# Kernel tuning notes

Measured on AMD Instinct MI355X. Metric: run time of the kernel, lower is better.

Reference implementation:

```python
import jax, jax.numpy as jnp
import numpy as np

NUM_TREES = 32
NUM_NODES = 6
SEED = 0
BATCH, CH, T = 16, 128, 4096


def _make_forest(num_trees, num_nodes, seed):
    """Random rooted trees: node 0 is root, node i>0 attaches to a uniform
    random earlier node (classic random recursive tree). Returns, per tree,
    the children-list representation."""
    rng = np.random.default_rng(seed)
    forest = []
    for _ in range(num_trees):
        children = [[] for _ in range(num_nodes)]
        for i in range(1, num_nodes):
            p = int(rng.integers(0, i))
            children[p].append(i)
        forest.append(children)
    return forest


def _excl_cumsum(u):
    # sum_{s < t} u[..., s]  (exclusive prefix sum along the ordered axis)
    return jnp.cumsum(u, axis=-1) - u


def _sum_trees(x, alphas, forest):
    """Iterated-sums evaluation over a forest in the (plus, times) semiring.
    Node value: v_i(t) = alpha_i * x(t) * prod_{c in children(i)} sum_{s<t} v_c(s).
    Tree output: sum_t v_root(t), per channel. x: [B,C,T]. Returns [B,num_trees,C]."""
    outs = []
    for t_idx, children in enumerate(forest):
        vals = {}
        for i in reversed(range(len(children))):  # leaves-to-root order
            v = alphas[t_idx, i][None, :, None] * x  # [B,C,T]
            for c in children[i]:
                v = v * _excl_cumsum(vals.pop(c))
            vals[i] = v
        outs.append(jnp.sum(vals[0], axis=-1))  # [B,C]
    return jnp.stack(outs, axis=1)  # [B,num_trees,C]


def setup_inputs() -> dict:
    key = jax.random.key(0)
    k1, k2 = jax.random.split(key)
    x = jax.random.normal(k1, (BATCH, CH, T), dtype=jnp.float32)
    alphas = jax.random.normal(k2, (NUM_TREES, NUM_NODES, CH), dtype=jnp.float32)
    return {"x": x, "alphas": alphas}


def reference(x, alphas):
    forest = _make_forest(NUM_TREES, NUM_NODES, SEED)
    return _sum_trees(x, alphas, forest)
```

## Files before the change

kernel.cpp:

```cpp
#include <hip/hip_runtime.h>
#include <cstdint>
#include <cstddef>

namespace cx {

constexpr uint32_t hashmix(uint32_t value, uint32_t& hc) {
    value ^= hc; hc *= 0x931e8875u; value *= hc; value ^= value >> 16; return value;
}
constexpr uint32_t mixf(uint32_t x, uint32_t y) {
    uint32_t r = x * 0xca01f9ddu - y * 0x4973f715u; r ^= r >> 16; return r;
}

struct Pcg64 {
    unsigned __int128 state{}, inc{};
    bool has_uint32{}; uint32_t uinteger{};
    static constexpr unsigned __int128 mult() {
        return (((unsigned __int128)2549297995355413924ULL) << 64) | 4865540595714422341ULL;
    }
    constexpr void step() { state = state * mult() + inc; }
    constexpr void seed_default0() {
        uint32_t pool[4] = {0, 0, 0, 0};
        uint32_t hc = 0x43b0d7e5u;
        for (int i = 0; i < 4; ++i) pool[i] = hashmix(0u, hc);
        for (int isrc = 0; isrc < 4; ++isrc)
            for (int idst = 0; idst < 4; ++idst)
                if (isrc != idst) pool[idst] = mixf(pool[idst], hashmix(pool[isrc], hc));
        uint32_t st[8] = {};
        uint32_t hc2 = 0x8b51f9ddu;
        for (int i = 0; i < 8; ++i) {
            uint32_t dv = pool[i & 3];
            dv ^= hc2; hc2 *= 0x58f38dedu; dv *= hc2; dv ^= dv >> 16;
            st[i] = dv;
        }
        const uint64_t v0 = (uint64_t)st[0] | ((uint64_t)st[1] << 32);
        const uint64_t v1 = (uint64_t)st[2] | ((uint64_t)st[3] << 32);
        const uint64_t v2 = (uint64_t)st[4] | ((uint64_t)st[5] << 32);
        const uint64_t v3 = (uint64_t)st[6] | ((uint64_t)st[7] << 32);
        const unsigned __int128 s = (((unsigned __int128)v0) << 64) | v1;
        const unsigned __int128 i_ = (((unsigned __int128)v2) << 64) | v3;
        state = 0; inc = (i_ << 1) | 1;
        step(); state += s; step();
        has_uint32 = false; uinteger = 0;
    }
    constexpr uint64_t next64() {
        step();
        const uint64_t hi = (uint64_t)(state >> 64), lo = (uint64_t)state;
        const uint64_t x = hi ^ lo;
        const unsigned rot = (unsigned)(state >> 122);
        return (x >> rot) | (x << ((64u - rot) & 63u));
    }
    constexpr uint32_t next32() {
        if (has_uint32) { has_uint32 = false; return uinteger; }
        const uint64_t n = next64();
        has_uint32 = true; uinteger = (uint32_t)(n >> 32);
        return (uint32_t)n;
    }
    constexpr uint32_t bounded_lemire32(uint32_t rng) {
        const uint32_t rng_excl = rng + 1u;
        uint64_t m = (uint64_t)next32() * (uint64_t)rng_excl;
        uint32_t leftover = (uint32_t)m;
        if (leftover < rng_excl) {
            const uint32_t threshold = (0xFFFFFFFFu - rng) % rng_excl;
            while (leftover < threshold) {
                m = (uint64_t)next32() * (uint64_t)rng_excl;
                leftover = (uint32_t)m;
            }
        }
        return (uint32_t)(m >> 32);
    }
    constexpr int64_t integers0(int64_t high) {
        const uint64_t rng = (uint64_t)(high - 1);
        if (rng == 0) return 0;
        return (int64_t)bounded_lemire32((uint32_t)rng);
    }
};

constexpr int NTREE = 32, MAXSER = 32, MAXROOT = 32, MAXFAC = 5, MAXSLOT = 12;

struct Plan {
    int nser, nroot, nslot, maxlvl;
    int lvl[MAXSER];
    int slot[MAXSER];
    int nfac[MAXSER];
    int fac[MAXSER][4];
    int rnfac[MAXROOT];
    int rfac[MAXROOT][MAXFAC];
    int rlvl[MAXROOT];
    int tree_root[NTREE];
};

constexpr Plan build_plan() {
    Plan P{};
    unsigned skey[MAXSER] = {}, rkey[MAXROOT] = {};
    P.nser = 1; skey[0] = (2u << 16) | 2u;
    P.nfac[0] = 0;
    P.nroot = 0;

    Pcg64 rng; rng.seed_default0();
    for (int t = 0; t < NTREE; ++t) {
        int par[6] = {0, 0, 0, 0, 0, 0};
        for (int i = 1; i <= 5; ++i) par[i] = (int)rng.integers0(i);
        int ch[6][5] = {}; int nch[6] = {};
        for (int i = 1; i <= 5; ++i) ch[par[i]][nch[par[i]]++] = i;

        int sid[6] = {}; unsigned keyn[6] = {};
        for (int i = 5; i >= 1; --i) {
            const int n = nch[i];
            unsigned ck[5] = {}; int cf[5] = {};
            for (int k = 0; k < n; ++k) { ck[k] = keyn[ch[i][k]]; cf[k] = sid[ch[i][k]]; }
            for (int a = 0; a < n; ++a)
                for (int bq = a + 1; bq < n; ++bq) {
                    if (ck[bq] > ck[a]) { unsigned tmp = ck[a]; ck[a] = ck[bq]; ck[bq] = tmp; }
                    if (cf[bq] < cf[a]) { int tmp = cf[a]; cf[a] = cf[bq]; cf[bq] = tmp; }
                }
            unsigned bits = 1u, len = 1u;
            for (int k = 0; k < n; ++k) { bits = (bits << (ck[k] >> 16)) | (ck[k] & 0xffffu); len += ck[k] >> 16; }
            bits <<= 1; len += 1;
            const unsigned key = (len << 16) | bits;
            keyn[i] = key;
            int id = -1;
            for (int q = 0; q < P.nser; ++q) if (skey[q] == key) { id = q; break; }
            if (id < 0) {
                id = P.nser++;
                skey[id] = key; P.nfac[id] = n;
                for (int k = 0; k < n; ++k) P.fac[id][k] = cf[k];
            }
            sid[i] = id;
        }
        {
            const int n = nch[0];
            unsigned ck[5] = {}; int cf[5] = {};
            for (int k = 0; k < n; ++k) { ck[k] = keyn[ch[0][k]]; cf[k] = sid[ch[0][k]]; }
            for (int a = 0; a < n; ++a)
                for (int bq = a + 1; bq < n; ++bq) {
                    if (ck[bq] > ck[a]) { unsigned tmp = ck[a]; ck[a] = ck[bq]; ck[bq] = tmp; }
                    if (cf[bq] < cf[a]) { int tmp = cf[a]; cf[a] = cf[bq]; cf[bq] = tmp; }
                }
            unsigned bits = 1u, len = 1u;
            for (int k = 0; k < n; ++k) { bits = (bits << (ck[k] >> 16)) | (ck[k] & 0xffffu); len += ck[k] >> 16; }
            bits <<= 1; len += 1;
            const unsigned key = (len << 16) | bits;
            int id = -1;
            for (int q = 0; q < P.nroot; ++q) if (rkey[q] == key) { id = q; break; }
            if (id < 0) {
                id = P.nroot++;
                rkey[id] = key; P.rnfac[id] = n;
                for (int k = 0; k < n; ++k) P.rfac[id][k] = cf[k];
            }
            P.tree_root[t] = id;
        }
    }
    P.lvl[0] = 0; P.maxlvl = 0;
    for (int s = 1; s < P.nser; ++s) {
        int m = 0;
        for (int k = 0; k < P.nfac[s]; ++k) { const int l = P.lvl[P.fac[s][k]]; if (l > m) m = l; }
        P.lvl[s] = m + 1;
        if (m + 1 > P.maxlvl) P.maxlvl = m + 1;
    }
    for (int r = 0; r < P.nroot; ++r) {
        int m = 0;
        for (int k = 0; k < P.rnfac[r]; ++k) { const int l = P.lvl[P.rfac[r][k]]; if (l > m) m = l; }
        P.rlvl[r] = m;
    }
    int last[MAXSER] = {};
    for (int s = 0; s < P.nser; ++s) last[s] = 0;
    for (int s = 1; s < P.nser; ++s)
        for (int k = 0; k < P.nfac[s]; ++k) { const int f = P.fac[s][k]; if (P.lvl[s] > last[f]) last[f] = P.lvl[s]; }
    for (int r = 0; r < P.nroot; ++r)
        for (int k = 0; k < P.rnfac[r]; ++k) { const int f = P.rfac[r][k]; if (P.rlvl[r] > last[f]) last[f] = P.rlvl[r]; }
    int free_at[MAXSLOT] = {};
    for (int q = 0; q < MAXSLOT; ++q) free_at[q] = -1000;
    P.nslot = 0;
    for (int L = 0; L <= P.maxlvl; ++L)
        for (int s = 0; s < P.nser; ++s) {
            if (P.lvl[s] != L) continue;
            int pick = -1;
            for (int q = 0; q < MAXSLOT; ++q) if (free_at[q] <= L) { pick = q; break; }
            P.slot[s] = pick;
            free_at[pick] = last[s] + 1;
            if (pick + 1 > P.nslot) P.nslot = pick + 1;
        }
    return P;
}

constexpr Plan PL = build_plan();
static_assert(PL.nser <= MAXSER && PL.nroot <= MAXROOT, "plan overflow");
static_assert(PL.nslot <= MAXSLOT && PL.maxlvl <= 9, "plan overflow");
static_assert(PL.nslot >= 1 && PL.nser >= 1 && PL.nroot >= 1, "plan degenerate");

}

template <int CTRL, int RM, bool BC>
__device__ __forceinline__ float dppmov(float x) {
    return __builtin_bit_cast(float,
        __builtin_amdgcn_update_dpp(0, __builtin_bit_cast(int, x), CTRL, RM, 0xf, BC));
}
__device__ __forceinline__ float wave_incl_scan(float v) {
    v += dppmov<0x111, 0xf, true>(v);
    v += dppmov<0x112, 0xf, true>(v);
    v += dppmov<0x114, 0xf, true>(v);
    v += dppmov<0x118, 0xf, true>(v);
    v += dppmov<0x142, 0xa, false>(v);
    v += dppmov<0x143, 0xc, false>(v);
    return v;
}

struct OutMap { unsigned char m[32]; };

#define THREADS 256
#define ELEM 16
#define NWAVE 4

__global__ __launch_bounds__(THREADS) void fis_kernel(const float* __restrict__ x,
                                                      const float* __restrict__ alphas,
                                                      float* __restrict__ out,
                                                      const OutMap om) {
    using cx::PL;
    constexpr int NSER = PL.nser, NROOT = PL.nroot, NSLOT = PL.nslot, MAXL = PL.maxlvl;

    const int tid = threadIdx.x;
    const int lane = tid & 63;
    const int wv = tid >> 6;
    const int b = blockIdx.x >> 7;
    const int c = blockIdx.x & 127;

    __shared__ float s_w[NSER + NROOT][NWAVE];

    float xr[ELEM];
    {
        const float4* xv = reinterpret_cast<const float4*>(
            x + (((size_t)b << 7) + (size_t)c) * 4096 + (size_t)tid * ELEM);
#pragma unroll
        for (int j = 0; j < 4; ++j) {
            const float4 v = xv[j];
            xr[4 * j + 0] = v.x; xr[4 * j + 1] = v.y;
            xr[4 * j + 2] = v.z; xr[4 * j + 3] = v.w;
        }
    }

    float S[NSLOT][ELEM];
    float wex[cx::MAXSER];

#pragma unroll
    for (int L = 0; L <= MAXL; ++L) {
#pragma unroll
        for (int s = 0; s < NSER; ++s) {
            if (PL.lvl[s] != L) continue;
            const int ds = PL.slot[s];
            float run = 0.f;
            if (PL.nfac[s] == 0) {
#pragma unroll
                for (int j = 0; j < ELEM; ++j) { S[ds][j] = run; run += xr[j]; }
            } else {
                const int fl = PL.slot[PL.fac[s][PL.nfac[s] - 1]];
#pragma unroll
                for (int j = 0; j < ELEM; ++j) {
                    float t = xr[j];
#pragma unroll
                    for (int k = 0; k < 3; ++k)
                        if (k < PL.nfac[s] - 1) t *= S[PL.slot[PL.fac[s][k]]][j];
                    S[ds][j] = run;
                    run = __builtin_fmaf(t, S[fl][j], run);
                }
            }
            const float wi = wave_incl_scan(run);
            if (lane == 63) s_w[s][wv] = wi;
            wex[s] = wi - run;
        }
        __syncthreads();
#pragma unroll
        for (int s = 0; s < NSER; ++s) {
            if (PL.lvl[s] != L) continue;
            const int ds = PL.slot[s];
            float base = wex[s];
#pragma unroll
            for (int k = 0; k < NWAVE - 1; ++k)
                if (k < wv) base += s_w[s][k];
#pragma unroll
            for (int j = 0; j < ELEM; ++j) S[ds][j] += base;
        }
#pragma unroll
        for (int r = 0; r < NROOT; ++r) {
            if (PL.rlvl[r] != L) continue;
            const int fl = PL.slot[PL.rfac[r][PL.rnfac[r] - 1]];
            float a0 = 0.f, a1 = 0.f;
#pragma unroll
            for (int j = 0; j < ELEM; j += 2) {
                float t0 = xr[j + 0];
                float t1 = xr[j + 1];
#pragma unroll
                for (int k = 0; k < 4; ++k) {
                    if (k < PL.rnfac[r] - 1) {
                        const int fs = PL.slot[PL.rfac[r][k]];
                        t0 *= S[fs][j + 0];
                        t1 *= S[fs][j + 1];
                    }
                }
                a0 = __builtin_fmaf(t0, S[fl][j + 0], a0);
                a1 = __builtin_fmaf(t1, S[fl][j + 1], a1);
            }
            const float wr = wave_incl_scan(a0 + a1);
            if (lane == 63) s_w[NSER + r][wv] = wr;
        }
    }

    __syncthreads();
    if (tid < 32) {
        const int rid = om.m[tid];
        float T = 0.f;
#pragma unroll
        for (int k = 0; k < NWAVE; ++k) T += s_w[NSER + rid][k];
        const float* ap = alphas + tid * 768 + c;
        const float aprod = ap[0] * ap[128] * ap[256] * ap[384] * ap[512] * ap[640];
        out[(((size_t)b << 5) + (size_t)tid) * 128 + c] = aprod * T;
    }
}

extern "C" void kernel_launch(void* const* d_in, const int* in_sizes, int n_in,
                              void* d_out, int out_size, void* d_ws, size_t ws_size,
                              hipStream_t stream) {
    const float* x = (const float*)d_in[0];
    const float* alphas = (const float*)d_in[1];
    float* out = (float*)d_out;

    OutMap om;
    for (int t = 0; t < cx::NTREE; ++t) om.m[t] = (unsigned char)cx::PL.tree_root[t];

    fis_kernel<<<dim3(16 * 128), dim3(THREADS), 0, stream>>>(x, alphas, out, om);
}
```

Baseline: 19.44 us.

## Map one (batch,channel) row per wave with chunked scan and carries

Each wave now processes a whole 4096-element row in four sequential chunks, carrying prefix-sum state across chunks in registers. This replaces the cross-wave shared-memory exchange and the per-level __syncthreads with readlane-based carries. Root accumulations are reduced only once at the end rather than per level. The cost is serialized chunk latency per wave, a quarter as many blocks, and extra carry and accumulator registers.

```diff
diff --git a/kernel.cpp b/kernel.cpp
--- a/kernel.cpp
+++ b/kernel.cpp
@@ -209,7 +209,7 @@
 
 #define THREADS 256
 #define ELEM 16
-#define NWAVE 4
+#define NCHUNK 4
 
 __global__ __launch_bounds__(THREADS) void fis_kernel(const float* __restrict__ x,
                                                       const float* __restrict__ alphas,
@@ -221,98 +221,95 @@
     const int tid = threadIdx.x;
     const int lane = tid & 63;
     const int wv = tid >> 6;
-    const int b = blockIdx.x >> 7;
-    const int c = blockIdx.x & 127;
-
-    __shared__ float s_w[NSER + NROOT][NWAVE];
-
-    float xr[ELEM];
-    {
-        const float4* xv = reinterpret_cast<const float4*>(
-            x + (((size_t)b << 7) + (size_t)c) * 4096 + (size_t)tid * ELEM);
-#pragma unroll
-        for (int j = 0; j < 4; ++j) {
-            const float4 v = xv[j];
-            xr[4 * j + 0] = v.x; xr[4 * j + 1] = v.y;
-            xr[4 * j + 2] = v.z; xr[4 * j + 3] = v.w;
-        }
-    }
+    const int bc = (blockIdx.x << 2) | wv;
+    const int b = bc >> 7;
+    const int c = bc & 127;
+
+    __shared__ float s_T[4][cx::MAXROOT];
+
+    float carry[cx::MAXSER];
+    float acc[cx::MAXROOT];
+#pragma unroll
+    for (int s = 0; s < NSER; ++s) carry[s] = 0.f;
+#pragma unroll
+    for (int r = 0; r < NROOT; ++r) acc[r] = 0.f;
+
+    const float4* xbase = reinterpret_cast<const float4*>(
+        x + (size_t)bc * 4096 + (size_t)lane * ELEM);
 
     float S[NSLOT][ELEM];
-    float wex[cx::MAXSER];
-
-#pragma unroll
-    for (int L = 0; L <= MAXL; ++L) {
-#pragma unroll
-        for (int s = 0; s < NSER; ++s) {
-            if (PL.lvl[s] != L) continue;
-            const int ds = PL.slot[s];
-            float run = 0.f;
-            if (PL.nfac[s] == 0) {
-#pragma unroll
-                for (int j = 0; j < ELEM; ++j) { S[ds][j] = run; run += xr[j]; }
-            } else {
-                const int fl = PL.slot[PL.fac[s][PL.nfac[s] - 1]];
+
+#pragma unroll 1
+    for (int ch = 0; ch < NCHUNK; ++ch) {
+        float xr[ELEM];
+        {
+            const float4* xv = xbase + (size_t)ch * 256;
+#pragma unroll
+            for (int j = 0; j < 4; ++j) {
+                const float4 v = xv[j];
+                xr[4 * j + 0] = v.x; xr[4 * j + 1] = v.y;
+                xr[4 * j + 2] = v.z; xr[4 * j + 3] = v.w;
+            }
+        }
+#pragma unroll
+        for (int L = 0; L <= MAXL; ++L) {
+#pragma unroll
+            for (int s = 0; s < NSER; ++s) {
+                if (PL.lvl[s] != L) continue;
+                const int ds = PL.slot[s];
+                float run = 0.f;
+                if (PL.nfac[s] == 0) {
+#pragma unroll
+                    for (int j = 0; j < ELEM; ++j) { S[ds][j] = run; run += xr[j]; }
+                } else {
+                    const int fl = PL.slot[PL.fac[s][PL.nfac[s] - 1]];
+#pragma unroll
+                    for (int j = 0; j < ELEM; ++j) {
+                        float t = xr[j];
+#pragma unroll
+                        for (int k = 0; k < 3; ++k)
+                            if (k < PL.nfac[s] - 1) t *= S[PL.slot[PL.fac[s][k]]][j];
+                        S[ds][j] = run;
+                        run = __builtin_fmaf(t, S[fl][j], run);
+                    }
+                }
+                const float wi = wave_incl_scan(run);
+                const float tot = __builtin_bit_cast(float,
+                    __builtin_amdgcn_readlane(__builtin_bit_cast(int, wi), 63));
+                const float base = (wi - run) + carry[s];
+                carry[s] += tot;
+#pragma unroll
+                for (int j = 0; j < ELEM; ++j) S[ds][j] += base;
+            }
+#pragma unroll
+            for (int r = 0; r < NROOT; ++r) {
+                if (PL.rlvl[r] != L) continue;
+                const int fl = PL.slot[PL.rfac[r][PL.rnfac[r] - 1]];
+                float a = acc[r];
 #pragma unroll
                 for (int j = 0; j < ELEM; ++j) {
                     float t = xr[j];
 #pragma unroll
-                    for (int k = 0; k < 3; ++k)
-                        if (k < PL.nfac[s] - 1) t *= S[PL.slot[PL.fac[s][k]]][j];
-                    S[ds][j] = run;
-                    run = __builtin_fmaf(t, S[fl][j], run);
+                    for (int k = 0; k < 4; ++k)
+                        if (k < PL.rnfac[r] - 1) t *= S[PL.slot[PL.rfac[r][k]]][j];
+                    a = __builtin_fmaf(t, S[fl][j], a);
                 }
-            }
-            const float wi = wave_incl_scan(run);
-            if (lane == 63) s_w[s][wv] = wi;
-            wex[s] = wi - run;
-        }
-        __syncthreads();
-#pragma unroll
-        for (int s = 0; s < NSER; ++s) {
-            if (PL.lvl[s] != L) continue;
-            const int ds = PL.slot[s];
-            float base = wex[s];
-#pragma unroll
-            for (int k = 0; k < NWAVE - 1; ++k)
-                if (k < wv) base += s_w[s][k];
-#pragma unroll
-            for (int j = 0; j < ELEM; ++j) S[ds][j] += base;
-        }
-#pragma unroll
-        for (int r = 0; r < NROOT; ++r) {
-            if (PL.rlvl[r] != L) continue;
-            const int fl = PL.slot[PL.rfac[r][PL.rnfac[r] - 1]];
-            float a0 = 0.f, a1 = 0.f;
-#pragma unroll
-            for (int j = 0; j < ELEM; j += 2) {
-                float t0 = xr[j + 0];
-                float t1 = xr[j + 1];
-#pragma unroll
-                for (int k = 0; k < 4; ++k) {
-                    if (k < PL.rnfac[r] - 1) {
-                        const int fs = PL.slot[PL.rfac[r][k]];
-                        t0 *= S[fs][j + 0];
-                        t1 *= S[fs][j + 1];
-                    }
-                }
-                a0 = __builtin_fmaf(t0, S[fl][j + 0], a0);
-                a1 = __builtin_fmaf(t1, S[fl][j + 1], a1);
-            }
-            const float wr = wave_incl_scan(a0 + a1);
-            if (lane == 63) s_w[NSER + r][wv] = wr;
-        }
-    }
-
-    __syncthreads();
-    if (tid < 32) {
-        const int rid = om.m[tid];
-        float T = 0.f;
-#pragma unroll
-        for (int k = 0; k < NWAVE; ++k) T += s_w[NSER + rid][k];
-        const float* ap = alphas + tid * 768 + c;
+                acc[r] = a;
+            }
+        }
+    }
+
+#pragma unroll
+    for (int r = 0; r < NROOT; ++r) {
+        const float wr = wave_incl_scan(acc[r]);
+        if (lane == 63) s_T[wv][r] = wr;
+    }
+    if (lane < 32) {
+        const int rid = om.m[lane];
+        const float T = s_T[wv][rid];
+        const float* ap = alphas + lane * 768 + c;
         const float aprod = ap[0] * ap[128] * ap[256] * ap[384] * ap[512] * ap[640];
-        out[(((size_t)b << 5) + (size_t)tid) * 128 + c] = aprod * T;
+        out[(((size_t)b << 5) + (size_t)lane) * 128 + c] = aprod * T;
     }
 }
 
@@ -326,5 +323,5 @@
     OutMap om;
     for (int t = 0; t < cx::NTREE; ++t) om.m[t] = (unsigned char)cx::PL.tree_root[t];
 
-    fis_kernel<<<dim3(16 * 128), dim3(THREADS), 0, stream>>>(x, alphas, out, om);
-}
+    fis_kernel<<<dim3(16 * 128 / 4), dim3(THREADS), 0, stream>>>(x, alphas, out, om);
+}
```

New measurement: 21.50 us. 10.6% more time.
